# Performance work log

Hardware: AMD Instinct MI355X
Metric: run time of the kernel (lower is better)

Reference implementation:

```python
import jax, jax.numpy as jnp
import numpy as np

# Propagation forward (reference path), with:
#   pairwise_fn       = dot product over feature dim: scores[b,i,j] = <val[b,i], val[b,j]>
#   edge_compress_fn  = softsign(x) = x / (1 + |x|)
#   val_proj/state_proj = Identity, return_delta = True
# Output: concat(delta_val [B,N,D], delta_state [B,N,1]) -> [B,N,D+1]

B, N, D = 4, 4096, 256


def setup_inputs() -> dict:
    key = jax.random.key(0)
    k1, k2 = jax.random.split(key)
    val = jax.random.normal(k1, (B, N, D), dtype=jnp.float32)
    state = jax.random.normal(k2, (B, N), dtype=jnp.float32)
    return {"val": val, "state": state}


def reference(val, state):
    # pairwise scores over all node pairs: [B, N, N]
    scores = jnp.einsum("bid,bjd->bij", val, val)
    # softsign edge compression
    edges = scores / (1.0 + jnp.abs(scores))
    # delta_state[b,i] = sum_j edges[b,i,j] * state[b,j]
    delta_state = jnp.einsum("bij,bj->bi", edges, state)
    # delta_val[b,i,d] = sum_j edges[b,i,j] * val[b,j,d]
    delta_val = jnp.einsum("bij,bjd->bid", edges, val)
    return jnp.concatenate([delta_val, delta_state[..., None]], axis=-1)
```

## Files before the change

### kernel.cpp

```cpp
#include <hip/hip_runtime.h>
#include <stdint.h>

#define BATCH 4
#define NN 4096
#define DD 256
#define TI 128
#define TJ 64
#define JS 2
#define JRANGE (NN / JS)
#define NITER (JRANGE / TJ)

#define VS_OFF 0
#define VT_OFF 65536
#define P_OFF  131072
#define SS_OFF 147456
#define LDS_BYTES 147968

typedef __attribute__((ext_vector_type(8))) short bf16x8;
typedef __attribute__((ext_vector_type(4))) float f32x4;
typedef __attribute__((ext_vector_type(4))) float f4v;
typedef __attribute__((ext_vector_type(8))) short s8v;
typedef __attribute__((ext_vector_type(4))) short s4v;

__device__ __forceinline__ short f2bf(float f) {
    uint32_t u = __builtin_bit_cast(uint32_t, f);
    u = (u + 0x7fffu + ((u >> 16) & 1u)) >> 16;
    return (short)u;
}

__device__ __forceinline__ void g2l16(const void* g, void* l) {
    __builtin_amdgcn_global_load_lds((const __attribute__((address_space(1))) void*)g,
                                     (__attribute__((address_space(3))) void*)l, 16, 0, 0);
}
__device__ __forceinline__ void g2l4(const void* g, void* l) {
    __builtin_amdgcn_global_load_lds((const __attribute__((address_space(1))) void*)g,
                                     (__attribute__((address_space(3))) void*)l, 4, 0, 0);
}

__global__ void convert_k(const float* __restrict__ in, short* __restrict__ out) {
    const int n8 = (BATCH * NN * DD) / 8;
    int stride = gridDim.x * blockDim.x;
    for (int i = blockIdx.x * blockDim.x + threadIdx.x; i < n8; i += stride) {
        f4v a = ((const f4v*)in)[2 * i];
        f4v b = ((const f4v*)in)[2 * i + 1];
        s8v o;
        o[0] = f2bf(a[0]); o[1] = f2bf(a[1]); o[2] = f2bf(a[2]); o[3] = f2bf(a[3]);
        o[4] = f2bf(b[0]); o[5] = f2bf(b[1]); o[6] = f2bf(b[2]); o[7] = f2bf(b[3]);
        ((s8v*)out)[i] = o;
    }
}

__global__ __launch_bounds__(256) void transpose_k(const float* __restrict__ val,
                                                   short* __restrict__ vt) {
    __shared__ float tile[32][33];
    int b = blockIdx.z;
    int d0 = blockIdx.x * 32, n0 = blockIdx.y * 32;
    int tx = threadIdx.x, ty = threadIdx.y;
#pragma unroll
    for (int yy = ty; yy < 32; yy += 8)
        tile[yy][tx] = val[((size_t)b * NN + n0 + yy) * DD + d0 + tx];
    __syncthreads();
#pragma unroll
    for (int yy = ty; yy < 32; yy += 8)
        vt[((size_t)b * DD + d0 + yy) * NN + n0 + tx] = f2bf(tile[tx][yy]);
}

__global__ void __launch_bounds__(512, 2) prop_main(const short* __restrict__ vbf,
                                                    const short* __restrict__ vtbf,
                                                    const float* __restrict__ state,
                                                    float* __restrict__ part,
                                                    float* __restrict__ spart) {
    extern __shared__ char smem[];

    const int bid = blockIdx.x;
    const int js = bid & 1;
    const int rb = (bid >> 1) & 31;
    const int b = bid >> 6;
    const int tid = threadIdx.x;
    const int w = tid >> 6, lane = tid & 63;
    const int g = lane >> 4, c = lane & 15;
    const int ig = w & 3, jh = w >> 2;
    const int wr = w & 1, wd = w >> 1;
    const int r7 = c & 7;
    const int j0base = js * JRANGE;

    const int xE = ((((r7 >> 2) << 2) | (g ^ (r7 & 3))) << 4);
    const int xO = (((((r7 >> 2) ^ 1) << 2) | (g ^ (r7 & 3))) << 4);

    bf16x8 Bf[2][8];
    const size_t irowb = (size_t)b * NN + rb * TI + ig * 32;
#pragma unroll
    for (int m = 0; m < 2; ++m)
#pragma unroll
        for (int k = 0; k < 8; ++k)
            Bf[m][k] = *(const bf16x8*)(vbf + ((irowb + m * 16 + c) * DD + k * 32 + g * 8));

    f32x4 accO[4][4];
#pragma unroll
    for (int mt = 0; mt < 4; ++mt)
#pragma unroll
        for (int dt = 0; dt < 4; ++dt)
            accO[mt][dt] = (f32x4){0.f, 0.f, 0.f, 0.f};
    float vsum[2] = {0.f, 0.f};

    auto stage = [&](int t, int nb) {
        const int j0 = j0base + t * TJ;
        {
            char* dst = smem + VS_OFF + nb * 32768;
#pragma unroll
            for (int p = 0; p < 4; ++p) {
                int ch0 = p * 512 + w * 64;
                int ch = ch0 + lane;
                int row = ch >> 5, cir = ch & 31;
                g2l16(vbf + ((size_t)(b * NN + j0 + row) * DD + ((cir ^ (row & 7)) * 8)),
                      dst + ch0 * 16);
            }
        }
        {
            char* dst = smem + VT_OFF + nb * 32768;
#pragma unroll
            for (int p = 0; p < 4; ++p) {
                int ch0 = p * 512 + w * 64;
                int ch = ch0 + lane;
                int d = ch >> 3, cj = ch & 7;
                g2l16(vtbf + ((size_t)(b * DD + d) * NN + j0 + ((cj ^ (d & 7)) * 8)),
                      dst + ch0 * 16);
            }
        }
        if (w == 0) g2l4(state + b * NN + j0 + lane, smem + SS_OFF + nb * 256);
    };

    stage(0, 0);
    __syncthreads();
    int pb = 0;
    for (int t = 0; t < NITER; ++t) {
        const char* VsB = smem + VS_OFF + pb * 32768;
        const char* VtB = smem + VT_OFF + pb * 32768;
        const char* SsB = smem + SS_OFF + pb * 256;

        f32x4 accS[2][2];
#pragma unroll
        for (int jbl = 0; jbl < 2; ++jbl)
#pragma unroll
            for (int m = 0; m < 2; ++m)
                accS[jbl][m] = (f32x4){0.f, 0.f, 0.f, 0.f};

        const char* aRow0 = VsB + (jh * 32 + c) * 512;
#pragma unroll
        for (int k = 0; k < 8; ++k) {
            const int off = (k >> 1) * 128 + ((k & 1) ? xO : xE);
            bf16x8 a0 = *(const bf16x8*)(aRow0 + off);
            bf16x8 a1 = *(const bf16x8*)(aRow0 + 8192 + off);
            accS[0][0] = __builtin_amdgcn_mfma_f32_16x16x32_bf16(a0, Bf[0][k], accS[0][0], 0, 0, 0);
            accS[0][1] = __builtin_amdgcn_mfma_f32_16x16x32_bf16(a0, Bf[1][k], accS[0][1], 0, 0, 0);
            accS[1][0] = __builtin_amdgcn_mfma_f32_16x16x32_bf16(a1, Bf[0][k], accS[1][0], 0, 0, 0);
            accS[1][1] = __builtin_amdgcn_mfma_f32_16x16x32_bf16(a1, Bf[1][k], accS[1][1], 0, 0, 0);
        }

#pragma unroll
        for (int jbl = 0; jbl < 2; ++jbl) {
            f4v sv = *(const f4v*)(SsB + (jh * 32 + jbl * 16 + g * 4) * 4);
#pragma unroll
            for (int m = 0; m < 2; ++m) {
                s4v pk;
#pragma unroll
                for (int r = 0; r < 4; ++r) {
                    float s = accS[jbl][m][r];
                    float e = s * __builtin_amdgcn_rcpf(1.0f + __builtin_fabsf(s));
                    vsum[m] += e * sv[r];
                    pk[r] = f2bf(e);
                }
                int i = ig * 32 + m * 16 + c;
                *(s4v*)(smem + P_OFF + i * 128 + ((jh * 64 + jbl * 32 + g * 8) ^ (r7 << 4))) = pk;
            }
        }

        __syncthreads();
        if (t + 1 < NITER) stage(t + 1, pb ^ 1);

        const char* paRow = smem + P_OFF + (wr * 64 + c) * 128;
        const char* vbRow = VtB + (wd * 64 + c) * 128;
#pragma unroll
        for (int kk = 0; kk < 2; ++kk) {
            const int off = kk ? xO : xE;
            bf16x8 pa[4], vb[4];
#pragma unroll
            for (int mt = 0; mt < 4; ++mt) pa[mt] = *(const bf16x8*)(paRow + mt * 2048 + off);
#pragma unroll
            for (int dt = 0; dt < 4; ++dt) vb[dt] = *(const bf16x8*)(vbRow + dt * 2048 + off);
#pragma unroll
            for (int mt = 0; mt < 4; ++mt)
#pragma unroll
                for (int dt = 0; dt < 4; ++dt)
                    accO[mt][dt] = __builtin_amdgcn_mfma_f32_16x16x32_bf16(pa[mt], vb[dt], accO[mt][dt], 0, 0, 0);
        }

        __syncthreads();
        pb ^= 1;
    }

    {
        float* po = part + (((size_t)(js * BATCH + b) * NN + rb * TI + wr * 64) * DD) + wd * 64;
#pragma unroll
        for (int mt = 0; mt < 4; ++mt)
#pragma unroll
            for (int dt = 0; dt < 4; ++dt)
#pragma unroll
                for (int r = 0; r < 4; ++r)
                    po[(size_t)(mt * 16 + g * 4 + r) * DD + dt * 16 + c] = accO[mt][dt][r];
    }

#pragma unroll
    for (int m = 0; m < 2; ++m) {
        vsum[m] += __shfl_xor(vsum[m], 16);
        vsum[m] += __shfl_xor(vsum[m], 32);
    }
    float* Xf = (float*)(smem + P_OFF);
    if (jh == 1 && lane < 16) {
        Xf[(ig * 2 + 0) * 16 + lane] = vsum[0];
        Xf[(ig * 2 + 1) * 16 + lane] = vsum[1];
    }
    __syncthreads();
    if (jh == 0 && lane < 16) {
        size_t sb = ((size_t)js * BATCH + b) * NN + rb * TI + ig * 32;
#pragma unroll
        for (int m = 0; m < 2; ++m)
            spart[sb + m * 16 + lane] = vsum[m] + Xf[(ig * 2 + m) * 16 + lane];
    }
}

__global__ __launch_bounds__(256) void reduce2_k(const float* __restrict__ part,
                                                 const float* __restrict__ spart,
                                                 float* __restrict__ out) {
    const int row = blockIdx.x;
    const int t = threadIdx.x;
    const size_t PS = (size_t)BATCH * NN * DD;
    float v = part[(size_t)row * DD + t] + part[PS + (size_t)row * DD + t];
    out[(size_t)row * 257 + t] = v;
    if (t == 0) {
        const size_t SS = (size_t)BATCH * NN;
        out[(size_t)row * 257 + 256] = spart[row] + spart[SS + row];
    }
}

extern "C" void kernel_launch(void* const* d_in, const int* in_sizes, int n_in,
                              void* d_out, int out_size, void* d_ws, size_t ws_size,
                              hipStream_t stream) {
    const float* val = (const float*)d_in[0];
    const float* state = (const float*)d_in[1];
    float* out = (float*)d_out;

    const size_t bf_bytes = (size_t)BATCH * NN * DD * 2;
    const size_t part_bytes = (size_t)JS * BATCH * NN * DD * 4;
    const size_t spart_bytes = (size_t)JS * BATCH * NN * 4;
    short* vbf = (short*)d_ws;
    short* vtbf = (short*)((char*)d_ws + bf_bytes);
    float* part = (float*)((char*)d_ws + 2 * bf_bytes);
    float* spart = (float*)((char*)d_ws + 2 * bf_bytes + part_bytes);
    if (ws_size < 2 * bf_bytes + part_bytes + spart_bytes) return;

    hipFuncSetAttribute((const void*)prop_main, hipFuncAttributeMaxDynamicSharedMemorySize, LDS_BYTES);

    convert_k<<<1024, 256, 0, stream>>>(val, vbf);
    transpose_k<<<dim3(DD / 32, NN / 32, BATCH), dim3(32, 8), 0, stream>>>(val, vtbf);
    prop_main<<<BATCH * (NN / TI) * JS, 512, LDS_BYTES, stream>>>(vbf, vtbf, state, part, spart);
    reduce2_k<<<BATCH * NN, 256, 0, stream>>>(part, spart, out);
}
```

Baseline: 101.5 us.

## Software-pipeline PV matmul one step behind scores and fuse prep kernels

Restructures the main loop so the P·V MFMA step for the previous tile runs after the score MFMAs of the current tile, with P double-buffered and a single barrier per iteration. V and V^T staging are split and issued at different points, and the PV step gets raised wave priority. State values are now read directly from global memory instead of staged through LDS. The separate convert and transpose kernels are merged into one prep kernel that writes both bf16 layouts. In exchange, LDS use grows to 160 KB, which may limit blocks per CU to one.

```diff
diff --git a/kernel.cpp b/kernel.cpp
--- a/kernel.cpp
+++ b/kernel.cpp
@@ -13,8 +13,7 @@
 #define VS_OFF 0
 #define VT_OFF 65536
 #define P_OFF  131072
-#define SS_OFF 147456
-#define LDS_BYTES 147968
+#define LDS_BYTES 163840
 
 typedef __attribute__((ext_vector_type(8))) short bf16x8;
 typedef __attribute__((ext_vector_type(4))) float f32x4;
@@ -32,33 +31,20 @@
     __builtin_amdgcn_global_load_lds((const __attribute__((address_space(1))) void*)g,
                                      (__attribute__((address_space(3))) void*)l, 16, 0, 0);
 }
-__device__ __forceinline__ void g2l4(const void* g, void* l) {
-    __builtin_amdgcn_global_load_lds((const __attribute__((address_space(1))) void*)g,
-                                     (__attribute__((address_space(3))) void*)l, 4, 0, 0);
-}
-
-__global__ void convert_k(const float* __restrict__ in, short* __restrict__ out) {
-    const int n8 = (BATCH * NN * DD) / 8;
-    int stride = gridDim.x * blockDim.x;
-    for (int i = blockIdx.x * blockDim.x + threadIdx.x; i < n8; i += stride) {
-        f4v a = ((const f4v*)in)[2 * i];
-        f4v b = ((const f4v*)in)[2 * i + 1];
-        s8v o;
-        o[0] = f2bf(a[0]); o[1] = f2bf(a[1]); o[2] = f2bf(a[2]); o[3] = f2bf(a[3]);
-        o[4] = f2bf(b[0]); o[5] = f2bf(b[1]); o[6] = f2bf(b[2]); o[7] = f2bf(b[3]);
-        ((s8v*)out)[i] = o;
-    }
-}
-
-__global__ __launch_bounds__(256) void transpose_k(const float* __restrict__ val,
-                                                   short* __restrict__ vt) {
+
+__global__ __launch_bounds__(256) void prep_k(const float* __restrict__ val,
+                                              short* __restrict__ vbf,
+                                              short* __restrict__ vt) {
     __shared__ float tile[32][33];
     int b = blockIdx.z;
     int d0 = blockIdx.x * 32, n0 = blockIdx.y * 32;
     int tx = threadIdx.x, ty = threadIdx.y;
 #pragma unroll
-    for (int yy = ty; yy < 32; yy += 8)
-        tile[yy][tx] = val[((size_t)b * NN + n0 + yy) * DD + d0 + tx];
+    for (int yy = ty; yy < 32; yy += 8) {
+        float v = val[((size_t)b * NN + n0 + yy) * DD + d0 + tx];
+        tile[yy][tx] = v;
+        vbf[((size_t)b * NN + n0 + yy) * DD + d0 + tx] = f2bf(v);
+    }
     __syncthreads();
 #pragma unroll
     for (int yy = ty; yy < 32; yy += 8)
@@ -103,40 +89,65 @@
             accO[mt][dt] = (f32x4){0.f, 0.f, 0.f, 0.f};
     float vsum[2] = {0.f, 0.f};
 
-    auto stage = [&](int t, int nb) {
+    auto stageVs = [&](int t, int nb) {
         const int j0 = j0base + t * TJ;
-        {
-            char* dst = smem + VS_OFF + nb * 32768;
-#pragma unroll
-            for (int p = 0; p < 4; ++p) {
-                int ch0 = p * 512 + w * 64;
-                int ch = ch0 + lane;
-                int row = ch >> 5, cir = ch & 31;
-                g2l16(vbf + ((size_t)(b * NN + j0 + row) * DD + ((cir ^ (row & 7)) * 8)),
-                      dst + ch0 * 16);
-            }
-        }
-        {
-            char* dst = smem + VT_OFF + nb * 32768;
-#pragma unroll
-            for (int p = 0; p < 4; ++p) {
-                int ch0 = p * 512 + w * 64;
-                int ch = ch0 + lane;
-                int d = ch >> 3, cj = ch & 7;
-                g2l16(vtbf + ((size_t)(b * DD + d) * NN + j0 + ((cj ^ (d & 7)) * 8)),
-                      dst + ch0 * 16);
-            }
-        }
-        if (w == 0) g2l4(state + b * NN + j0 + lane, smem + SS_OFF + nb * 256);
+        char* dst = smem + VS_OFF + nb * 32768;
+#pragma unroll
+        for (int p = 0; p < 4; ++p) {
+            int ch0 = p * 512 + w * 64;
+            int ch = ch0 + lane;
+            int row = ch >> 5, cir = ch & 31;
+            g2l16(vbf + ((size_t)(b * NN + j0 + row) * DD + ((cir ^ (row & 7)) * 8)),
+                  dst + ch0 * 16);
+        }
     };
-
-    stage(0, 0);
-    __syncthreads();
-    int pb = 0;
+    auto stageVt = [&](int t, int nb) {
+        const int j0 = j0base + t * TJ;
+        char* dst = smem + VT_OFF + nb * 32768;
+#pragma unroll
+        for (int p = 0; p < 4; ++p) {
+            int ch0 = p * 512 + w * 64;
+            int ch = ch0 + lane;
+            int d = ch >> 3, cj = ch & 7;
+            g2l16(vtbf + ((size_t)(b * DD + d) * NN + j0 + ((cj ^ (d & 7)) * 8)),
+                  dst + ch0 * 16);
+        }
+    };
+
+    auto pvStep = [&](int slot) {
+        const char* paRow = smem + P_OFF + slot * 16384 + (wr * 64 + c) * 128;
+        const char* vbRow = smem + VT_OFF + slot * 32768 + (wd * 64 + c) * 128;
+        __builtin_amdgcn_s_setprio(1);
+#pragma unroll
+        for (int kk = 0; kk < 2; ++kk) {
+            const int off = kk ? xO : xE;
+            bf16x8 pa[4], vb[4];
+#pragma unroll
+            for (int mt = 0; mt < 4; ++mt) pa[mt] = *(const bf16x8*)(paRow + mt * 2048 + off);
+#pragma unroll
+            for (int dt = 0; dt < 4; ++dt) vb[dt] = *(const bf16x8*)(vbRow + dt * 2048 + off);
+#pragma unroll
+            for (int mt = 0; mt < 4; ++mt)
+#pragma unroll
+                for (int dt = 0; dt < 4; ++dt)
+                    accO[mt][dt] = __builtin_amdgcn_mfma_f32_16x16x32_bf16(pa[mt], vb[dt], accO[mt][dt], 0, 0, 0);
+        }
+        __builtin_amdgcn_s_setprio(0);
+    };
+
+    const float* stp = state + b * NN + j0base;
+
+    stageVs(0, 0);
+    stageVt(0, 0);
+    __syncthreads();
+
     for (int t = 0; t < NITER; ++t) {
-        const char* VsB = smem + VS_OFF + pb * 32768;
-        const char* VtB = smem + VT_OFF + pb * 32768;
-        const char* SsB = smem + SS_OFF + pb * 256;
+        const int cur = t & 1, prv = cur ^ 1;
+
+        if (t + 1 < NITER) stageVs(t + 1, prv);
+
+        f4v sv0 = *(const f4v*)(stp + t * TJ + jh * 32 + g * 4);
+        f4v sv1 = *(const f4v*)(stp + t * TJ + jh * 32 + 16 + g * 4);
 
         f32x4 accS[2][2];
 #pragma unroll
@@ -145,7 +156,7 @@
             for (int m = 0; m < 2; ++m)
                 accS[jbl][m] = (f32x4){0.f, 0.f, 0.f, 0.f};
 
-        const char* aRow0 = VsB + (jh * 32 + c) * 512;
+        const char* aRow0 = smem + VS_OFF + cur * 32768 + (jh * 32 + c) * 512;
 #pragma unroll
         for (int k = 0; k < 8; ++k) {
             const int off = (k >> 1) * 128 + ((k & 1) ? xO : xE);
@@ -157,9 +168,11 @@
             accS[1][1] = __builtin_amdgcn_mfma_f32_16x16x32_bf16(a1, Bf[1][k], accS[1][1], 0, 0, 0);
         }
 
+        if (t > 0) pvStep(prv);
+
 #pragma unroll
         for (int jbl = 0; jbl < 2; ++jbl) {
-            f4v sv = *(const f4v*)(SsB + (jh * 32 + jbl * 16 + g * 4) * 4);
+            f4v sv = jbl ? sv1 : sv0;
 #pragma unroll
             for (int m = 0; m < 2; ++m) {
                 s4v pk;
@@ -171,33 +184,17 @@
                     pk[r] = f2bf(e);
                 }
                 int i = ig * 32 + m * 16 + c;
-                *(s4v*)(smem + P_OFF + i * 128 + ((jh * 64 + jbl * 32 + g * 8) ^ (r7 << 4))) = pk;
+                *(s4v*)(smem + P_OFF + cur * 16384 + i * 128 +
+                        ((jh * 64 + jbl * 32 + g * 8) ^ (r7 << 4))) = pk;
             }
         }
 
         __syncthreads();
-        if (t + 1 < NITER) stage(t + 1, pb ^ 1);
-
-        const char* paRow = smem + P_OFF + (wr * 64 + c) * 128;
-        const char* vbRow = VtB + (wd * 64 + c) * 128;
-#pragma unroll
-        for (int kk = 0; kk < 2; ++kk) {
-            const int off = kk ? xO : xE;
-            bf16x8 pa[4], vb[4];
-#pragma unroll
-            for (int mt = 0; mt < 4; ++mt) pa[mt] = *(const bf16x8*)(paRow + mt * 2048 + off);
-#pragma unroll
-            for (int dt = 0; dt < 4; ++dt) vb[dt] = *(const bf16x8*)(vbRow + dt * 2048 + off);
-#pragma unroll
-            for (int mt = 0; mt < 4; ++mt)
-#pragma unroll
-                for (int dt = 0; dt < 4; ++dt)
-                    accO[mt][dt] = __builtin_amdgcn_mfma_f32_16x16x32_bf16(pa[mt], vb[dt], accO[mt][dt], 0, 0, 0);
-        }
-
-        __syncthreads();
-        pb ^= 1;
-    }
+
+        if (t + 1 < NITER) stageVt(t + 1, prv);
+    }
+
+    pvStep((NITER - 1) & 1);
 
     {
         float* po = part + (((size_t)(js * BATCH + b) * NN + rb * TI + wr * 64) * DD) + wd * 64;
@@ -216,6 +213,7 @@
         vsum[m] += __shfl_xor(vsum[m], 32);
     }
     float* Xf = (float*)(smem + P_OFF);
+    __syncthreads();
     if (jh == 1 && lane < 16) {
         Xf[(ig * 2 + 0) * 16 + lane] = vsum[0];
         Xf[(ig * 2 + 1) * 16 + lane] = vsum[1];
@@ -261,8 +259,7 @@
 
     hipFuncSetAttribute((const void*)prop_main, hipFuncAttributeMaxDynamicSharedMemorySize, LDS_BYTES);
 
-    convert_k<<<1024, 256, 0, stream>>>(val, vbf);
-    transpose_k<<<dim3(DD / 32, NN / 32, BATCH), dim3(32, 8), 0, stream>>>(val, vtbf);
+    prep_k<<<dim3(DD / 32, NN / 32, BATCH), dim3(32, 8), 0, stream>>>(val, vbf, vtbf);
     prop_main<<<BATCH * (NN / TI) * JS, 512, LDS_BYTES, stream>>>(vbf, vtbf, state, part, spart);
     reduce2_k<<<BATCH * NN, 256, 0, stream>>>(part, spart, out);
 }
```

New measurement: 93.38 us. 8.0% less time.
